# Performance work log

Hardware: AMD Instinct MI355X
Metric: run time of the kernel (lower is better)

Reference implementation:

```python
import jax, jax.numpy as jnp
import numpy as np

B, L, LE = 2, 1024, 1024
NM, DM, NL = 80, 512, 8
LAYERS = NL // 2
DS, EXP, K, H = 16, 2, 4, 4
DI = EXP * DM            # 1024
DTR = (DM + 15) // 16    # dt_rank 'auto' -> 32
HD = DM // H             # 128


def setup_inputs() -> dict:
    key = jax.random.key(0)
    ks = iter(jax.random.split(key, 48))
    n = lambda shape, s=0.02: jax.random.normal(next(ks), shape, jnp.float32) * s
    return {
        "x": jax.random.normal(next(ks), (B, L, NM), jnp.float32),
        "enc_output": jax.random.normal(next(ks), (B, LE, DM), jnp.float32),
        "W_in": n((DM, NM)), "b_in": jnp.zeros((DM,), jnp.float32),
        "m_norm_w": jnp.ones((LAYERS, DM), jnp.float32),
        "m_in_w": n((LAYERS, 2 * DI, DM)),
        "m_conv_w": n((LAYERS, DI, K), 0.1),
        "m_conv_b": jnp.zeros((LAYERS, DI), jnp.float32),
        "m_xproj_w": n((LAYERS, DTR + 2 * DS, DI)),
        "m_dt_w": n((LAYERS, DI, DTR)),
        "m_dt_b": n((LAYERS, DI), 0.1),
        "m_Alog": jnp.tile(jnp.log(jnp.arange(1, DS + 1, dtype=jnp.float32))[None, None, :], (LAYERS, DI, 1)),
        "m_D": jnp.ones((LAYERS, DI), jnp.float32),
        "m_out_w": n((LAYERS, DM, DI)),
        "a_in_w": n((LAYERS, 3 * DM, DM)),
        "a_in_b": jnp.zeros((LAYERS, 3 * DM), jnp.float32),
        "a_out_w": n((LAYERS, DM, DM)),
        "a_out_b": jnp.zeros((LAYERS, DM), jnp.float32),
        "a_ln_w": jnp.ones((LAYERS, DM), jnp.float32),
        "a_ln_b": jnp.zeros((LAYERS, DM), jnp.float32),
        "normf_w": jnp.ones((DM,), jnp.float32),
        "W_out": n((NM, DM)),
    }


def rmsnorm(x, w, eps=1e-5):
    return x * jax.lax.rsqrt(jnp.mean(x * x, axis=-1, keepdims=True) + eps) * w


def layernorm(x, w, b, eps=1e-5):
    m = jnp.mean(x, axis=-1, keepdims=True)
    v = jnp.mean((x - m) ** 2, axis=-1, keepdims=True)
    return (x - m) * jax.lax.rsqrt(v + eps) * w + b


def dwconv_causal(x, w, b):
    # x: (B,L,DI), w: (DI,K) depthwise; torch Conv1d(padding=K-1)[..., :L] == left-pad K-1
    xt = jnp.transpose(x, (0, 2, 1))  # (B,DI,L)
    y = jax.lax.conv_general_dilated(xt, w[:, None, :], (1,), [(K - 1, 0)],
                                     feature_group_count=DI,
                                     dimension_numbers=("NCH", "OIH", "NCH"))
    return jnp.transpose(y, (0, 2, 1)) + b


def selective_scan_cumsum(u, delta, A, Bm, Cm, Dv):
    # mamba-tiny 'cumsum' scan. u,delta: (B,L,DI); A: (DI,DS); Bm,Cm: (B,L,DS); Dv: (DI,)
    dA = jnp.einsum("bld,dn->bldn", delta, A)
    dBu = jnp.einsum("bld,bld,bln->bldn", delta, u, Bm)
    shifted = jnp.pad(dA[:, 1:], ((0, 0), (0, 1), (0, 0), (0, 0)))
    dA_cs = jnp.exp(jnp.flip(jnp.cumsum(jnp.flip(shifted, 1), 1), 1))  # suffix-sum exp
    xs = jnp.cumsum(dBu * dA_cs, axis=1) / (dA_cs + 1e-12)
    y = jnp.einsum("bldn,bln->bld", xs, Cm)
    return y + u * Dv


def mamba_block(u, in_w, conv_w, conv_b, xproj_w, dt_w, dt_b, Alog, Dv, out_w):
    xr = u @ in_w.T                       # (B,L,2*DI)
    xm, res = xr[..., :DI], xr[..., DI:]
    xm = jax.nn.silu(dwconv_causal(xm, conv_w, conv_b))
    x_dbl = xm @ xproj_w.T                # (B,L,DTR+2*DS)
    dlt = x_dbl[..., :DTR]
    Bm = x_dbl[..., DTR:DTR + DS]
    Cm = x_dbl[..., DTR + DS:]
    delta = jax.nn.softplus(dlt @ dt_w.T + dt_b)
    A = -jnp.exp(Alog)
    y = selective_scan_cumsum(xm, delta, A, Bm, Cm, Dv)
    y = y * jax.nn.silu(res)
    return y @ out_w.T


def cross_attn_block(q_in, kv, in_w, in_b, out_w, out_b, ln_w, ln_b):
    Wq, Wk, Wv = in_w[:DM], in_w[DM:2 * DM], in_w[2 * DM:]
    bq, bk, bv = in_b[:DM], in_b[DM:2 * DM], in_b[2 * DM:]
    q = (q_in @ Wq.T + bq).reshape(B, -1, H, HD)
    k = (kv @ Wk.T + bk).reshape(B, -1, H, HD)
    v = (kv @ Wv.T + bv).reshape(B, -1, H, HD)
    scores = jnp.einsum("bqhd,bkhd->bhqk", q, k) / jnp.sqrt(jnp.float32(HD))
    attn = jax.nn.softmax(scores, axis=-1)
    o = jnp.einsum("bhqk,bkhd->bqhd", attn, v).reshape(B, -1, DM)
    o = o @ out_w.T + out_b
    return layernorm(q_in + o, ln_w, ln_b)  # dropout is identity in eval


def reference(x, enc_output, W_in, b_in, m_norm_w, m_in_w, m_conv_w, m_conv_b,
              m_xproj_w, m_dt_w, m_dt_b, m_Alog, m_D, m_out_w,
              a_in_w, a_in_b, a_out_w, a_out_b, a_ln_w, a_ln_b, normf_w, W_out):
    h = x @ W_in.T + b_in
    for i in range(LAYERS):
        h = h + mamba_block(rmsnorm(h, m_norm_w[i]), m_in_w[i], m_conv_w[i],
                            m_conv_b[i], m_xproj_w[i], m_dt_w[i], m_dt_b[i],
                            m_Alog[i], m_D[i], m_out_w[i])
        h = cross_attn_block(h, enc_output, a_in_w[i], a_in_b[i],
                             a_out_w[i], a_out_b[i], a_ln_w[i], a_ln_b[i])
    h = rmsnorm(h, normf_w)
    return h @ W_out.T
```

## Files before the change

### kernel.cpp

```cpp
#include <hip/hip_runtime.h>
#include <hip/hip_bf16.h>
#include <math.h>

typedef __hip_bfloat16 bf16;
typedef __attribute__((ext_vector_type(8))) short short8x;
typedef __attribute__((ext_vector_type(4))) float f32x4;

static constexpr int cB   = 2;
static constexpr int cL   = 1024;
static constexpr int cLE  = 1024;
static constexpr int cNM  = 80;
static constexpr int cDM  = 512;
static constexpr int cLAYERS = 4;
static constexpr int cDS  = 16;
static constexpr int cKC  = 4;
static constexpr int cH   = 4;
static constexpr int cDI  = 1024;
static constexpr int cDTR = 32;
static constexpr int cHD  = 128;

static constexpr int cNCH = 64;
static constexpr int cCHL = cL / cNCH;

#define GLL16(g, l) __builtin_amdgcn_global_load_lds( \
    (const __attribute__((address_space(1))) void*)(g), \
    (__attribute__((address_space(3))) void*)(l), 16, 0, 0)

template<int ACT, int BM, int BN>
__global__ __launch_bounds__(256)
void bgemm_kernel(const bf16* __restrict__ A, const bf16* __restrict__ W,
                  const float* __restrict__ bias, const float* __restrict__ addv,
                  float* __restrict__ Cf, bf16* __restrict__ Cb,
                  int M, int N, int Kd, int lda, int ldw, int ldcf, int ldcb, int ldadd,
                  int bdiv, long sA1, long sA2, long sW1, long sW2,
                  long sCf1, long sCf2, long sCb1, long sCb2)
{
    constexpr int RM = BM / 32;
    constexpr int RN = BN / 32;
    const int z = blockIdx.z;
    const int i1 = z / bdiv, i2 = z % bdiv;
    A += i1 * sA1 + i2 * sA2;
    W += i1 * sW1 + i2 * sW2;

    const int bm = blockIdx.y * BM;
    const int bn = blockIdx.x * BN;
    const int tid = threadIdx.x;
    const int lane = tid & 63;
    const int wid = tid >> 6;
    const int wr = wid >> 1, wc = wid & 1;

    __shared__ bf16 As[BM * 32];
    __shared__ bf16 Bs[BN * 32];

    f32x4 acc[RM][RN] = {};

    const int r_in = lane >> 2;
    const int kb   = (lane & 3) * 8;
    const int hi   = lane >> 4;
    const int rc   = lane & 15;

    for (int k0 = 0; k0 < Kd; k0 += 32) {
#pragma unroll
        for (int iss = 0; iss < BM / 64; iss++) {
            const int row = wid * (BM / 4) + iss * 16 + r_in;
            int gm = bm + row; if (gm >= M) gm = M - 1;
            const bf16* ga = A + (long)gm * lda + k0 + kb;
            GLL16(ga, As + (wid * (BM / 4) + iss * 16) * 32);
        }
#pragma unroll
        for (int iss = 0; iss < BN / 64; iss++) {
            const int row = wid * (BN / 4) + iss * 16 + r_in;
            int gn = bn + row; if (gn >= N) gn = N - 1;
            const bf16* gb = W + (long)gn * ldw + k0 + kb;
            GLL16(gb, Bs + (wid * (BN / 4) + iss * 16) * 32);
        }
        asm volatile("s_waitcnt vmcnt(0)" ::: "memory");
        __syncthreads();

        short8x af[RM], bfv[RN];
#pragma unroll
        for (int i = 0; i < RM; i++)
            af[i] = *(const short8x*)(As + (wr * (BM / 2) + i * 16 + rc) * 32 + hi * 8);
#pragma unroll
        for (int j = 0; j < RN; j++)
            bfv[j] = *(const short8x*)(Bs + (wc * (BN / 2) + j * 16 + rc) * 32 + hi * 8);
#pragma unroll
        for (int i = 0; i < RM; i++)
#pragma unroll
            for (int j = 0; j < RN; j++)
                acc[i][j] = __builtin_amdgcn_mfma_f32_16x16x32_bf16(af[i], bfv[j], acc[i][j], 0, 0, 0);
        __syncthreads();
    }

    const long cfo = i1 * sCf1 + i2 * sCf2;
    const long cbo = i1 * sCb1 + i2 * sCb2;
#pragma unroll
    for (int i = 0; i < RM; i++) {
#pragma unroll
        for (int r = 0; r < 4; r++) {
            const int gm = bm + wr * (BM / 2) + i * 16 + hi * 4 + r;
            if (gm >= M) continue;
#pragma unroll
            for (int j = 0; j < RN; j++) {
                const int gn = bn + wc * (BN / 2) + j * 16 + rc;
                if (gn >= N) continue;
                float v = acc[i][j][r];
                if (bias) v += bias[gn];
                if (ACT == 1) v = (v > 20.f) ? v : log1pf(__expf(v));
                if (addv) v += addv[cfo + (long)gm * ldadd + gn];
                if (Cf) Cf[cfo + (long)gm * ldcf + gn] = v;
                if (Cb) Cb[cbo + (long)gm * ldcb + gn] = __float2bfloat16(v);
            }
        }
    }
}

static inline void bgemm(int ACT, int BM, int BN, const bf16* A, const bf16* W, const float* bias,
                         const float* addv, float* Cf, bf16* Cb,
                         int M, int N, int Kd, int lda, int ldw, int ldcf, int ldcb, int ldadd,
                         int nz, int bdiv, long sA1, long sA2, long sW1, long sW2,
                         long sCf1, long sCf2, long sCb1, long sCb2, hipStream_t s)
{
    dim3 g((N + BN - 1) / BN, (M + BM - 1) / BM, nz), b(256);
#define BG_ARGS A, W, bias, addv, Cf, Cb, M, N, Kd, lda, ldw, ldcf, ldcb, ldadd, \
                bdiv, sA1, sA2, sW1, sW2, sCf1, sCf2, sCb1, sCb2
    if (BM == 128) {
        if (ACT == 1) bgemm_kernel<1, 128, 128><<<g, b, 0, s>>>(BG_ARGS);
        else          bgemm_kernel<0, 128, 128><<<g, b, 0, s>>>(BG_ARGS);
    } else if (BN == 128) {
        if (ACT == 1) bgemm_kernel<1, 64, 128><<<g, b, 0, s>>>(BG_ARGS);
        else          bgemm_kernel<0, 64, 128><<<g, b, 0, s>>>(BG_ARGS);
    } else {
        bgemm_kernel<0, 64, 64><<<g, b, 0, s>>>(BG_ARGS);
    }
#undef BG_ARGS
}

static inline void bgemm_plain(int ACT, int BM, int BN, const bf16* A, const bf16* W,
                               const float* bias, const float* addv, float* Cf, bf16* Cb,
                               int M, int N, int Kd, int lda, int ldw, int ldcf, int ldcb,
                               int ldadd, hipStream_t s)
{
    bgemm(ACT, BM, BN, A, W, bias, addv, Cf, Cb, M, N, Kd, lda, ldw, ldcf, ldcb, ldadd,
          1, 1, 0, 0, 0, 0, 0, 0, 0, 0, s);
}

__global__ __launch_bounds__(128)
void flash_attn_kernel(const bf16* __restrict__ Qp, const bf16* __restrict__ Kp,
                       const bf16* __restrict__ VTp, bf16* __restrict__ Op, float scale)
{
    const int qt = blockIdx.x;
    const int bh = blockIdx.y;
    const int b = bh >> 2, h = bh & 3;
    const int tid = threadIdx.x;
    const int w = tid >> 6;
    const int lane = tid & 63;
    const int rc = lane & 15, hi = lane >> 4;
    const int rlo = rc & 7;

    __shared__ bf16 Qs[32 * 128];
    __shared__ bf16 Ks[64 * 128];
    __shared__ bf16 Vs[128 * 64];
    __shared__ bf16 Ps[32 * 64];

    {
        const bf16* qb = Qp + ((long)(b * cL + qt * 32)) * cDM + h * cHD;
#pragma unroll
        for (int c = 0; c < 4; c++) {
            const int row = w * 16 + c * 4 + (lane >> 4);
            const int gc = (lane & 15) ^ (row & 7);
            GLL16(qb + (long)row * cDM + gc * 8, Qs + (w * 16 + c * 4) * 128);
        }
    }
    asm volatile("s_waitcnt vmcnt(0)" ::: "memory");
    __syncthreads();

    short8x aq[4];
#pragma unroll
    for (int kk = 0; kk < 4; kk++) {
        const int sc = (kk * 4 + hi) ^ rlo;
        aq[kk] = *(const short8x*)(Qs + (w * 16 + rc) * 128 + sc * 8);
    }

    float m_r[4], l_r[4];
#pragma unroll
    for (int r = 0; r < 4; r++) { m_r[r] = -1e30f; l_r[r] = 0.f; }
    f32x4 oacc[8] = {};

    const bf16* kb0 = Kp + ((long)(b * cLE)) * (2 * cDM) + h * cHD;
    const bf16* vb0 = VTp + ((long)(b * cDM + h * cHD)) * cLE;

    for (int kt = 0; kt < 16; kt++) {
        __syncthreads();
#pragma unroll
        for (int c = 0; c < 8; c++) {
            const int row = w * 32 + c * 4 + (lane >> 4);
            const int gc = (lane & 15) ^ (row & 7);
            GLL16(kb0 + ((long)(kt * 64 + row)) * (2 * cDM) + gc * 8,
                  Ks + (w * 32 + c * 4) * 128);
        }
#pragma unroll
        for (int c = 0; c < 8; c++) {
            const int row = w * 64 + c * 8 + (lane >> 3);
            const int gc = (lane & 7) ^ (row & 7);
            GLL16(vb0 + (long)row * cLE + kt * 64 + gc * 8,
                  Vs + (w * 64 + c * 8) * 64);
        }
        asm volatile("s_waitcnt vmcnt(0)" ::: "memory");
        __syncthreads();

        f32x4 s[4] = {};
#pragma unroll
        for (int kk = 0; kk < 4; kk++) {
            const int sc = (kk * 4 + hi) ^ rlo;
#pragma unroll
            for (int j = 0; j < 4; j++) {
                short8x bk = *(const short8x*)(Ks + (j * 16 + rc) * 128 + sc * 8);
                s[j] = __builtin_amdgcn_mfma_f32_16x16x32_bf16(aq[kk], bk, s[j], 0, 0, 0);
            }
        }

        float p[4][4];
        float esc[4];
#pragma unroll
        for (int r = 0; r < 4; r++) {
            const float v0 = s[0][r] * scale, v1 = s[1][r] * scale;
            const float v2 = s[2][r] * scale, v3 = s[3][r] * scale;
            float mx = fmaxf(fmaxf(v0, v1), fmaxf(v2, v3));
            mx = fmaxf(mx, __shfl_xor(mx, 1));
            mx = fmaxf(mx, __shfl_xor(mx, 2));
            mx = fmaxf(mx, __shfl_xor(mx, 4));
            mx = fmaxf(mx, __shfl_xor(mx, 8));
            const float mn = fmaxf(m_r[r], mx);
            p[0][r] = __expf(v0 - mn);
            p[1][r] = __expf(v1 - mn);
            p[2][r] = __expf(v2 - mn);
            p[3][r] = __expf(v3 - mn);
            float rs = (p[0][r] + p[1][r]) + (p[2][r] + p[3][r]);
            rs += __shfl_xor(rs, 1);
            rs += __shfl_xor(rs, 2);
            rs += __shfl_xor(rs, 4);
            rs += __shfl_xor(rs, 8);
            esc[r] = __expf(m_r[r] - mn);
            l_r[r] = l_r[r] * esc[r] + rs;
            m_r[r] = mn;
        }
#pragma unroll
        for (int j2 = 0; j2 < 8; j2++)
#pragma unroll
            for (int r = 0; r < 4; r++)
                oacc[j2][r] *= esc[r];
#pragma unroll
        for (int j = 0; j < 4; j++)
#pragma unroll
            for (int r = 0; r < 4; r++) {
                const int q = w * 16 + hi * 4 + r;
                const int cp = (j * 2 + (rc >> 3)) ^ (q & 7);
                Ps[q * 64 + cp * 8 + (rc & 7)] = __float2bfloat16(p[j][r]);
            }
        __syncthreads();
#pragma unroll
        for (int ks = 0; ks < 2; ks++) {
            const int sc = (ks * 4 + hi) ^ rlo;
            short8x ap = *(const short8x*)(Ps + (w * 16 + rc) * 64 + sc * 8);
#pragma unroll
            for (int j2 = 0; j2 < 8; j2++) {
                short8x bv = *(const short8x*)(Vs + (j2 * 16 + rc) * 64 + sc * 8);
                oacc[j2] = __builtin_amdgcn_mfma_f32_16x16x32_bf16(ap, bv, oacc[j2], 0, 0, 0);
            }
        }
    }

    float inv[4];
#pragma unroll
    for (int r = 0; r < 4; r++) inv[r] = 1.f / l_r[r];
    bf16* ob = Op + ((long)(b * cL + qt * 32)) * cDM + h * cHD;
#pragma unroll
    for (int j2 = 0; j2 < 8; j2++)
#pragma unroll
        for (int r = 0; r < 4; r++)
            ob[(long)(w * 16 + hi * 4 + r) * cDM + j2 * 16 + rc] =
                __float2bfloat16(oacc[j2][r] * inv[r]);
}

__global__ void splitk_reduce_kernel(const float* __restrict__ parts, float* __restrict__ outf,
                                     bf16* __restrict__ outb, int n4, int sliceN4, int S)
{
    const int i = blockIdx.x * 256 + threadIdx.x;
    if (i >= n4) return;
    float4 a = ((const float4*)parts)[i];
    for (int s2 = 1; s2 < S; s2++) {
        float4 b2 = ((const float4*)parts)[i + (long)s2 * sliceN4];
        a.x += b2.x; a.y += b2.y; a.z += b2.z; a.w += b2.w;
    }
    ((float4*)outf)[i] = a;
    bf16 b0 = __float2bfloat16(a.x), b1 = __float2bfloat16(a.y);
    bf16 b2 = __float2bfloat16(a.z), b3 = __float2bfloat16(a.w);
    short4 pk = { *(short*)&b0, *(short*)&b1, *(short*)&b2, *(short*)&b3 };
    ((short4*)outb)[i] = pk;
}

__global__ void f32_to_bf16_kernel(const float* __restrict__ in, bf16* __restrict__ out, long n)
{
    long i = ((long)blockIdx.x * 256 + threadIdx.x) * 4;
    if (i + 3 < n) {
        float4 v = *(const float4*)(in + i);
        out[i]     = __float2bfloat16(v.x);
        out[i + 1] = __float2bfloat16(v.y);
        out[i + 2] = __float2bfloat16(v.z);
        out[i + 3] = __float2bfloat16(v.w);
    } else {
        for (; i < n; i++) out[i] = __float2bfloat16(in[i]);
    }
}
static inline void cvt(const float* in, bf16* out, long n, hipStream_t s)
{
    int blocks = (int)((n / 4 + 255) / 256);
    f32_to_bf16_kernel<<<blocks, 256, 0, s>>>(in, out, n);
}

__global__ void cvt_pad_kernel(const float* __restrict__ in, bf16* __restrict__ out,
                               int rows, int kin, int kout)
{
    const int idx = blockIdx.x * 256 + threadIdx.x;
    if (idx >= rows * kout) return;
    const int r = idx / kout, k = idx - r * kout;
    out[idx] = __float2bfloat16(k < kin ? in[(long)r * kin + k] : 0.f);
}

__global__ void transpose_bf16_kernel(const bf16* __restrict__ in, bf16* __restrict__ out,
                                      int ldin, int col0)
{
    __shared__ bf16 t[32][33];
    const int b = blockIdx.z;
    const int le0 = blockIdx.x * 32, d0 = blockIdx.y * 32;
    const int tid = threadIdx.x;
    const int c = tid & 31, r = tid >> 5;
    for (int i = r; i < 32; i += 8)
        t[i][c] = in[((long)b * cLE + le0 + i) * ldin + col0 + d0 + c];
    __syncthreads();
    for (int i = r; i < 32; i += 8)
        out[((long)b * cDM + d0 + i) * cLE + le0 + c] = t[c][i];
}

__global__ void rmsnorm_kernel(const float* __restrict__ x, const float* __restrict__ w,
                               float* __restrict__ outf, bf16* __restrict__ outb, int Dm)
{
    const int row = blockIdx.x;
    const float* xr = x + (long)row * Dm;
    float s = 0.f;
    for (int i = threadIdx.x; i < Dm; i += 256) { float v = xr[i]; s += v * v; }
    __shared__ float red[5];
    const int lane = threadIdx.x & 63, wv = threadIdx.x >> 6;
#pragma unroll
    for (int off = 1; off < 64; off <<= 1) s += __shfl_xor(s, off);
    if (lane == 0) red[wv] = s;
    __syncthreads();
    if (threadIdx.x == 0) {
        float t = red[0] + red[1] + red[2] + red[3];
        red[4] = rsqrtf(t / Dm + 1e-5f);
    }
    __syncthreads();
    const float scale = red[4];
    for (int i = threadIdx.x; i < Dm; i += 256) {
        float v = xr[i] * scale * w[i];
        if (outf) outf[(long)row * Dm + i] = v;
        if (outb) outb[(long)row * Dm + i] = __float2bfloat16(v);
    }
}

__global__ void layernorm_kernel(const float* __restrict__ x, const float* __restrict__ w,
                                 const float* __restrict__ b, float* __restrict__ outf,
                                 bf16* __restrict__ outb, int Dm)
{
    const int row = blockIdx.x;
    const float* xr = x + (long)row * Dm;
    float s = 0.f, sq = 0.f;
    for (int i = threadIdx.x; i < Dm; i += 256) { float v = xr[i]; s += v; sq += v * v; }
    __shared__ float red[8];
    __shared__ float mv[2];
    const int lane = threadIdx.x & 63, wv = threadIdx.x >> 6;
#pragma unroll
    for (int off = 1; off < 64; off <<= 1) { s += __shfl_xor(s, off); sq += __shfl_xor(sq, off); }
    if (lane == 0) { red[wv] = s; red[4 + wv] = sq; }
    __syncthreads();
    if (threadIdx.x == 0) {
        float ts = red[0] + red[1] + red[2] + red[3];
        float tq = red[4] + red[5] + red[6] + red[7];
        float m = ts / Dm;
        float var = tq / Dm - m * m;
        mv[0] = m;
        mv[1] = rsqrtf(var + 1e-5f);
    }
    __syncthreads();
    const float m = mv[0], rs = mv[1];
    for (int i = threadIdx.x; i < Dm; i += 256) {
        float v = (xr[i] - m) * rs * w[i] + b[i];
        outf[(long)row * Dm + i] = v;
        outb[(long)row * Dm + i] = __float2bfloat16(v);
    }
}

__global__ void conv_silu_kernel(const float* __restrict__ xr, const float* __restrict__ w,
                                 const float* __restrict__ bias, float* __restrict__ xm,
                                 bf16* __restrict__ xmb)
{
    const int idx = blockIdx.x * 256 + threadIdx.x;
    if (idx >= cB * cL * cDI) return;
    const int d = idx & (cDI - 1);
    const int l = (idx >> 10) & (cL - 1);
    const int b = idx >> 20;
    float s = bias[d];
#pragma unroll
    for (int j = 0; j < cKC; j++) {
        const int ls = l + j - (cKC - 1);
        if (ls >= 0) s += w[d * cKC + j] * xr[((long)(b * cL + ls)) * (2 * cDI) + d];
    }
    s = s / (1.f + __expf(-s));
    xm[(long)idx] = s;
    xmb[(long)idx] = __float2bfloat16(s);
}

__global__ void scan_phase1(const float* __restrict__ xm, const float* __restrict__ delta,
                            const float* __restrict__ xdbl, const float* __restrict__ Alog,
                            float* __restrict__ aprod_out, float* __restrict__ send_out)
{
    const int idx4 = blockIdx.x * 256 + threadIdx.x;
    const int ng = idx4 & 3;
    const int d  = (idx4 >> 2) & (cDI - 1);
    const int ch = (idx4 >> 12) & (cNCH - 1);
    const int b  = idx4 >> 18;
    const float4 Al = *(const float4*)(Alog + d * cDS + 4 * ng);
    const float A0 = -__expf(Al.x), A1 = -__expf(Al.y), A2 = -__expf(Al.z), A3 = -__expf(Al.w);
    float s0 = 0.f, s1 = 0.f, s2 = 0.f, s3 = 0.f;
    float p0 = 1.f, p1 = 1.f, p2 = 1.f, p3 = 1.f;
    const int l0 = ch * cCHL;
    const float* dp = delta + (long)(b * cL + l0) * cDI + d;
    const float* up = xm    + (long)(b * cL + l0) * cDI + d;
    const float* xb = xdbl  + (long)(b * cL + l0) * 64 + cDTR + 4 * ng;
#pragma unroll
    for (int t = 0; t < cCHL; t++) {
        const float dl = dp[(long)t * cDI];
        const float du = dl * up[(long)t * cDI];
        const float4 Bv = *(const float4*)(xb + (long)t * 64);
        const float a0 = __expf(dl * A0), a1 = __expf(dl * A1);
        const float a2 = __expf(dl * A2), a3 = __expf(dl * A3);
        s0 = a0 * s0 + du * Bv.x; p0 *= a0;
        s1 = a1 * s1 + du * Bv.y; p1 *= a1;
        s2 = a2 * s2 + du * Bv.z; p2 *= a2;
        s3 = a3 * s3 + du * Bv.w; p3 *= a3;
    }
    const long base4 = (((long)(b * cNCH + ch) * cDI + d) * cDS) + 4 * ng;
    float4 pv = { p0, p1, p2, p3 };
    float4 sv = { s0, s1, s2, s3 };
    *(float4*)(aprod_out + base4) = pv;
    *(float4*)(send_out + base4)  = sv;
}

__global__ void scan_phase2(const float* __restrict__ aprod, const float* __restrict__ send,
                            float* __restrict__ sinit)
{
    const int j = blockIdx.x * 256 + threadIdx.x;
    const int n = j & (cDS - 1);
    const int d = (j >> 4) & (cDI - 1);
    const int b = j >> 14;
    float s = 0.f;
#pragma unroll
    for (int c = 0; c < cNCH; c++) {
        const long off = (((long)(b * cNCH + c) * cDI + d) * cDS) + n;
        sinit[off] = s;
        s = aprod[off] * s + send[off];
    }
}

__global__ void scan_phase3(const float* __restrict__ xm, const float* __restrict__ delta,
                            const float* __restrict__ xdbl, const float* __restrict__ Alog,
                            const float* __restrict__ Dv, const float* __restrict__ xr,
                            const float* __restrict__ sinit, bf16* __restrict__ y)
{
    const int idx4 = blockIdx.x * 256 + threadIdx.x;
    const int ng = idx4 & 3;
    const int d  = (idx4 >> 2) & (cDI - 1);
    const int ch = (idx4 >> 12) & (cNCH - 1);
    const int b  = idx4 >> 18;
    const float4 Al = *(const float4*)(Alog + d * cDS + 4 * ng);
    const float A0 = -__expf(Al.x), A1 = -__expf(Al.y), A2 = -__expf(Al.z), A3 = -__expf(Al.w);
    const float Dval = Dv[d];
    const long base4 = (((long)(b * cNCH + ch) * cDI + d) * cDS) + 4 * ng;
    float4 st = *(const float4*)(sinit + base4);
    float s0 = st.x, s1 = st.y, s2 = st.z, s3 = st.w;
    const int l0 = ch * cCHL;
    const float* dp = delta + (long)(b * cL + l0) * cDI + d;
    const float* up = xm    + (long)(b * cL + l0) * cDI + d;
    const float* xb = xdbl  + (long)(b * cL + l0) * 64 + cDTR + 4 * ng;
    const float* xc = xb + cDS;
    const float* rp = xr + (long)(b * cL + l0) * (2 * cDI) + cDI + d;
    bf16* yp = y + (long)(b * cL + l0) * cDI + d;
#pragma unroll
    for (int t = 0; t < cCHL; t++) {
        const float dl = dp[(long)t * cDI];
        const float u  = up[(long)t * cDI];
        const float du = dl * u;
        const float4 Bv = *(const float4*)(xb + (long)t * 64);
        const float4 Cv = *(const float4*)(xc + (long)t * 64);
        const float a0 = __expf(dl * A0), a1 = __expf(dl * A1);
        const float a2 = __expf(dl * A2), a3 = __expf(dl * A3);
        s0 = a0 * s0 + du * Bv.x;
        s1 = a1 * s1 + du * Bv.y;
        s2 = a2 * s2 + du * Bv.z;
        s3 = a3 * s3 + du * Bv.w;
        float c = s0 * Cv.x;
        c = fmaf(s1, Cv.y, c);
        c = fmaf(s2, Cv.z, c);
        c = fmaf(s3, Cv.w, c);
        c += __shfl_xor(c, 1);
        c += __shfl_xor(c, 2);
        if (ng == 0) {
            const float res = rp[(long)t * 2 * cDI];
            const float sig = 1.f / (1.f + __expf(-res));
            yp[(long)t * cDI] = __float2bfloat16((c + u * Dval) * (res * sig));
        }
    }
}

extern "C" void kernel_launch(void* const* d_in, const int* in_sizes, int n_in,
                              void* d_out, int out_size, void* d_ws, size_t ws_size,
                              hipStream_t stream)
{
    const float* x       = (const float*)d_in[0];
    const float* enc     = (const float*)d_in[1];
    const float* W_in    = (const float*)d_in[2];
    const float* b_in    = (const float*)d_in[3];
    const float* m_norm_w= (const float*)d_in[4];
    const float* m_in_w  = (const float*)d_in[5];
    const float* m_conv_w= (const float*)d_in[6];
    const float* m_conv_b= (const float*)d_in[7];
    const float* m_xproj = (const float*)d_in[8];
    const float* m_dt_w  = (const float*)d_in[9];
    const float* m_dt_b  = (const float*)d_in[10];
    const float* m_Alog  = (const float*)d_in[11];
    const float* m_D     = (const float*)d_in[12];
    const float* m_out_w = (const float*)d_in[13];
    const float* a_in_w  = (const float*)d_in[14];
    const float* a_in_b  = (const float*)d_in[15];
    const float* a_out_w = (const float*)d_in[16];
    const float* a_out_b = (const float*)d_in[17];
    const float* a_ln_w  = (const float*)d_in[18];
    const float* a_ln_b  = (const float*)d_in[19];
    const float* normf_w = (const float*)d_in[20];
    const float* W_out   = (const float*)d_in[21];
    float* out = (float*)d_out;

    float* ws = (float*)d_ws;
    long off = 0;
    auto allocf = [&](long n) { float* p = ws + off; off += n; return p; };

    const long M1 = 1 << 20;
    float* bufH    = allocf(M1);
    float* bufPre  = allocf(M1);
    float* bufXR   = allocf(4 * M1);
    float* bufXM   = allocf(2 * M1);
    float* bufDelta= allocf(2 * M1);
    float* bufXDBL = allocf(M1 / 8);
    bf16* bufU    = (bf16*)allocf(M1 / 2);
    bf16* bufHb   = (bf16*)allocf(M1 / 2);
    bf16* bufXMb  = (bf16*)allocf(M1);
    bf16* bufXDBLb= (bf16*)allocf(M1 / 16);
    bf16* bufY    = (bf16*)allocf(M1);
    bf16* bufQ    = (bf16*)allocf(M1 / 2);
    bf16* bufKV   = (bf16*)allocf(M1);
    bf16* bufVT   = (bf16*)allocf(M1 / 2);
    bf16* bufO    = (bf16*)allocf(M1 / 2);
    bf16* encb    = (bf16*)allocf(M1 / 2);
    bf16* w_in_b  = (bf16*)allocf(2 * M1);
    bf16* w_xp_b  = (bf16*)allocf(M1 / 8);
    bf16* w_dt_b  = (bf16*)allocf(M1 / 16);
    bf16* w_out_b = (bf16*)allocf(M1);
    bf16* w_ain_b = (bf16*)allocf(3 * M1 / 2);
    bf16* w_aout_b= (bf16*)allocf(M1 / 2);
    bf16* x_pad   = (bf16*)allocf(2048L * 96 / 2);
    bf16* w_inp_b = (bf16*)allocf(512L * 96 / 2);
    bf16* w_outf_b= (bf16*)allocf(80L * 512 / 2);
    float* bufAP  = allocf(2 * M1);
    float* bufSE  = allocf(2 * M1);
    float* bufSI  = allocf(2 * M1);

    const int Mrows = cB * cL;
    const long SUMSZ4 = (long)cB * cNCH * cDI * 4;

    cvt(enc,      encb,    (long)cB * cLE * cDM, stream);
    cvt(m_in_w,   w_in_b,  (long)cLAYERS * 2 * cDI * cDM, stream);
    cvt(m_xproj,  w_xp_b,  (long)cLAYERS * 64 * cDI, stream);
    cvt(m_dt_w,   w_dt_b,  (long)cLAYERS * cDI * cDTR, stream);
    cvt(m_out_w,  w_out_b, (long)cLAYERS * cDM * cDI, stream);
    cvt(a_in_w,   w_ain_b, (long)cLAYERS * 3 * cDM * cDM, stream);
    cvt(a_out_w,  w_aout_b,(long)cLAYERS * cDM * cDM, stream);
    cvt(W_out,    w_outf_b,(long)cNM * cDM, stream);
    cvt_pad_kernel<<<(Mrows * 96 + 255) / 256, 256, 0, stream>>>(x, x_pad, Mrows, cNM, 96);
    cvt_pad_kernel<<<(cDM * 96 + 255) / 256, 256, 0, stream>>>(W_in, w_inp_b, cDM, cNM, 96);

    bgemm_plain(0, 64, 64, x_pad, w_inp_b, b_in, nullptr, bufH, nullptr,
                Mrows, cDM, 96, 96, 96, cDM, 0, 0, stream);

    for (int i = 0; i < cLAYERS; i++) {
        const float* norm_w = m_norm_w + (long)i * cDM;
        const bf16*  in_w   = w_in_b   + (long)i * 2 * cDI * cDM;
        const float* conv_w = m_conv_w + (long)i * cDI * cKC;
        const float* conv_b = m_conv_b + (long)i * cDI;
        const bf16*  xproj  = w_xp_b   + (long)i * 64 * cDI;
        const bf16*  dt_w   = w_dt_b   + (long)i * cDI * cDTR;
        const float* dt_b   = m_dt_b   + (long)i * cDI;
        const float* Alog   = m_Alog   + (long)i * cDI * cDS;
        const float* Dv     = m_D      + (long)i * cDI;
        const bf16*  out_w  = w_out_b  + (long)i * cDM * cDI;
        const bf16*  ain_w  = w_ain_b  + (long)i * 3 * cDM * cDM;
        const float* ain_b  = a_in_b   + (long)i * 3 * cDM;
        const bf16*  aout_w = w_aout_b + (long)i * cDM * cDM;
        const float* aout_b = a_out_b  + (long)i * cDM;
        const float* ln_w   = a_ln_w   + (long)i * cDM;
        const float* ln_b   = a_ln_b   + (long)i * cDM;

        rmsnorm_kernel<<<Mrows, 256, 0, stream>>>(bufH, norm_w, nullptr, bufU, cDM);
        bgemm_plain(0, 64, 128, bufU, in_w, nullptr, nullptr, bufXR, nullptr,
                    Mrows, 2 * cDI, cDM, cDM, cDM, 2 * cDI, 0, 0, stream);
        conv_silu_kernel<<<(cB * cL * cDI) / 256, 256, 0, stream>>>(bufXR, conv_w, conv_b, bufXM, bufXMb);
        bgemm(0, 64, 64, bufXMb, xproj, nullptr, nullptr, bufPre, nullptr,
              Mrows, 64, cDI / 8, cDI, cDI, 64, 0, 0,
              8, 1, 128, 0, 128, 0, (long)Mrows * 64, 0, 0, 0, stream);
        splitk_reduce_kernel<<<(Mrows * 64 / 4 + 255) / 256, 256, 0, stream>>>(
            bufPre, bufXDBL, bufXDBLb, Mrows * 64 / 4, Mrows * 64 / 4, 8);
        bgemm_plain(1, 64, 128, bufXDBLb, dt_w, dt_b, nullptr, bufDelta, nullptr,
                    Mrows, cDI, cDTR, 64, cDTR, cDI, 0, 0, stream);
        scan_phase1<<<(int)(SUMSZ4 / 256), 256, 0, stream>>>(bufXM, bufDelta, bufXDBL, Alog, bufAP, bufSE);
        scan_phase2<<<(cB * cDI * cDS) / 256, 256, 0, stream>>>(bufAP, bufSE, bufSI);
        scan_phase3<<<(int)(SUMSZ4 / 256), 256, 0, stream>>>(bufXM, bufDelta, bufXDBL, Alog, Dv, bufXR, bufSI, bufY);
        bgemm_plain(0, 64, 64, bufY, out_w, nullptr, bufH, bufH, bufHb,
                    Mrows, cDM, cDI, cDI, cDI, cDM, cDM, cDM, stream);

        bgemm_plain(0, 64, 64, bufHb, ain_w, ain_b, nullptr, nullptr, bufQ,
                    Mrows, cDM, cDM, cDM, cDM, 0, cDM, 0, stream);
        bgemm_plain(0, 64, 128, encb, ain_w + (long)cDM * cDM, ain_b + cDM, nullptr, nullptr, bufKV,
                    Mrows, 2 * cDM, cDM, cDM, cDM, 0, 2 * cDM, 0, stream);
        {
            dim3 g(cLE / 32, cDM / 32, cB);
            transpose_bf16_kernel<<<g, 256, 0, stream>>>(bufKV, bufVT, 2 * cDM, cDM);
        }
        {
            dim3 g(cL / 32, cB * cH);
            flash_attn_kernel<<<g, 128, 0, stream>>>(bufQ, bufKV, bufVT, bufO,
                                                     0.08838834764831845f);
        }
        bgemm_plain(0, 64, 64, bufO, aout_w, aout_b, bufH, bufPre, nullptr,
                    Mrows, cDM, cDM, cDM, cDM, cDM, 0, cDM, stream);
        layernorm_kernel<<<Mrows, 256, 0, stream>>>(bufPre, ln_w, ln_b, bufH, bufHb, cDM);
    }

    rmsnorm_kernel<<<Mrows, 256, 0, stream>>>(bufH, normf_w, nullptr, bufU, cDM);
    bgemm_plain(0, 64, 64, bufU, w_outf_b, nullptr, nullptr, out, nullptr,
                Mrows, cNM, cDM, cDM, cDM, cNM, 0, 0, stream);
}
```

Before: 858.7 us.

## Batch K/V projections for all layers upfront and merge weight conversions

```diff
diff --git a/kernel.cpp b/kernel.cpp
--- a/kernel.cpp
+++ b/kernel.cpp
@@ -33,7 +33,7 @@
                   float* __restrict__ Cf, bf16* __restrict__ Cb,
                   int M, int N, int Kd, int lda, int ldw, int ldcf, int ldcb, int ldadd,
                   int bdiv, long sA1, long sA2, long sW1, long sW2,
-                  long sCf1, long sCf2, long sCb1, long sCb2)
+                  long sCf1, long sCf2, long sCb1, long sCb2, long sBias)
 {
     constexpr int RM = BM / 32;
     constexpr int RN = BN / 32;
@@ -41,6 +41,7 @@
     const int i1 = z / bdiv, i2 = z % bdiv;
     A += i1 * sA1 + i2 * sA2;
     W += i1 * sW1 + i2 * sW2;
+    if (bias) bias += i1 * sBias;
 
     const int bm = blockIdx.y * BM;
     const int bn = blockIdx.x * BN;
@@ -119,11 +120,11 @@
                          const float* addv, float* Cf, bf16* Cb,
                          int M, int N, int Kd, int lda, int ldw, int ldcf, int ldcb, int ldadd,
                          int nz, int bdiv, long sA1, long sA2, long sW1, long sW2,
-                         long sCf1, long sCf2, long sCb1, long sCb2, hipStream_t s)
+                         long sCf1, long sCf2, long sCb1, long sCb2, long sBias, hipStream_t s)
 {
     dim3 g((N + BN - 1) / BN, (M + BM - 1) / BM, nz), b(256);
 #define BG_ARGS A, W, bias, addv, Cf, Cb, M, N, Kd, lda, ldw, ldcf, ldcb, ldadd, \
-                bdiv, sA1, sA2, sW1, sW2, sCf1, sCf2, sCb1, sCb2
+                bdiv, sA1, sA2, sW1, sW2, sCf1, sCf2, sCb1, sCb2, sBias
     if (BM == 128) {
         if (ACT == 1) bgemm_kernel<1, 128, 128><<<g, b, 0, s>>>(BG_ARGS);
         else          bgemm_kernel<0, 128, 128><<<g, b, 0, s>>>(BG_ARGS);
@@ -142,7 +143,7 @@
                                int ldadd, hipStream_t s)
 {
     bgemm(ACT, BM, BN, A, W, bias, addv, Cf, Cb, M, N, Kd, lda, ldw, ldcf, ldcb, ldadd,
-          1, 1, 0, 0, 0, 0, 0, 0, 0, 0, s);
+          1, 1, 0, 0, 0, 0, 0, 0, 0, 0, 0, s);
 }
 
 __global__ __launch_bounds__(128)
@@ -300,23 +301,36 @@
     ((short4*)outb)[i] = pk;
 }
 
-__global__ void f32_to_bf16_kernel(const float* __restrict__ in, bf16* __restrict__ out, long n)
-{
+__global__ void cvt_all_kernel(
+    const float* __restrict__ s0, bf16* __restrict__ d0,
+    const float* __restrict__ s1, bf16* __restrict__ d1,
+    const float* __restrict__ s2, bf16* __restrict__ d2,
+    const float* __restrict__ s3, bf16* __restrict__ d3,
+    const float* __restrict__ s4, bf16* __restrict__ d4,
+    const float* __restrict__ s5, bf16* __restrict__ d5,
+    const float* __restrict__ s6, bf16* __restrict__ d6,
+    const float* __restrict__ s7, bf16* __restrict__ d7)
+{
+    constexpr long E0 = 1048576, E1 = 4194304, E2 = 262144, E3 = 131072;
+    constexpr long E4 = 2097152, E5 = 3145728, E6 = 1048576, E7 = 40960;
+    constexpr long C0 = E0, C1 = C0 + E1, C2 = C1 + E2, C3 = C2 + E3;
+    constexpr long C4 = C3 + E4, C5 = C4 + E5, C6 = C5 + E6, C7 = C6 + E7;
     long i = ((long)blockIdx.x * 256 + threadIdx.x) * 4;
-    if (i + 3 < n) {
-        float4 v = *(const float4*)(in + i);
-        out[i]     = __float2bfloat16(v.x);
-        out[i + 1] = __float2bfloat16(v.y);
-        out[i + 2] = __float2bfloat16(v.z);
-        out[i + 3] = __float2bfloat16(v.w);
-    } else {
-        for (; i < n; i++) out[i] = __float2bfloat16(in[i]);
-    }
-}
-static inline void cvt(const float* in, bf16* out, long n, hipStream_t s)
-{
-    int blocks = (int)((n / 4 + 255) / 256);
-    f32_to_bf16_kernel<<<blocks, 256, 0, s>>>(in, out, n);
+    if (i >= C7) return;
+    const float* s; bf16* d;
+    if      (i < C0) { s = s0; d = d0; }
+    else if (i < C1) { s = s1; d = d1; i -= C0; }
+    else if (i < C2) { s = s2; d = d2; i -= C1; }
+    else if (i < C3) { s = s3; d = d3; i -= C2; }
+    else if (i < C4) { s = s4; d = d4; i -= C3; }
+    else if (i < C5) { s = s5; d = d5; i -= C4; }
+    else if (i < C6) { s = s6; d = d6; i -= C5; }
+    else             { s = s7; d = d7; i -= C6; }
+    float4 v = *(const float4*)(s + i);
+    d[i]     = __float2bfloat16(v.x);
+    d[i + 1] = __float2bfloat16(v.y);
+    d[i + 2] = __float2bfloat16(v.z);
+    d[i + 3] = __float2bfloat16(v.w);
 }
 
 __global__ void cvt_pad_kernel(const float* __restrict__ in, bf16* __restrict__ out,
@@ -329,10 +343,13 @@
 }
 
 __global__ void transpose_bf16_kernel(const bf16* __restrict__ in, bf16* __restrict__ out,
-                                      int ldin, int col0)
+                                      int ldin, int col0, long inLS, long outLS)
 {
     __shared__ bf16 t[32][33];
-    const int b = blockIdx.z;
+    const int z = blockIdx.z;
+    const int lay = z >> 1, b = z & 1;
+    in  += (long)lay * inLS;
+    out += (long)lay * outLS;
     const int le0 = blockIdx.x * 32, d0 = blockIdx.y * 32;
     const int tid = threadIdx.x;
     const int c = tid & 31, r = tid >> 5;
@@ -568,8 +585,6 @@
     bf16* bufXDBLb= (bf16*)allocf(M1 / 16);
     bf16* bufY    = (bf16*)allocf(M1);
     bf16* bufQ    = (bf16*)allocf(M1 / 2);
-    bf16* bufKV   = (bf16*)allocf(M1);
-    bf16* bufVT   = (bf16*)allocf(M1 / 2);
     bf16* bufO    = (bf16*)allocf(M1 / 2);
     bf16* encb    = (bf16*)allocf(M1 / 2);
     bf16* w_in_b  = (bf16*)allocf(2 * M1);
@@ -584,20 +599,32 @@
     float* bufAP  = allocf(2 * M1);
     float* bufSE  = allocf(2 * M1);
     float* bufSI  = allocf(2 * M1);
+    bf16* bufKV4  = (bf16*)allocf(4 * M1);
+    bf16* bufVT4  = (bf16*)allocf(2 * M1);
 
     const int Mrows = cB * cL;
     const long SUMSZ4 = (long)cB * cNCH * cDI * 4;
-
-    cvt(enc,      encb,    (long)cB * cLE * cDM, stream);
-    cvt(m_in_w,   w_in_b,  (long)cLAYERS * 2 * cDI * cDM, stream);
-    cvt(m_xproj,  w_xp_b,  (long)cLAYERS * 64 * cDI, stream);
-    cvt(m_dt_w,   w_dt_b,  (long)cLAYERS * cDI * cDTR, stream);
-    cvt(m_out_w,  w_out_b, (long)cLAYERS * cDM * cDI, stream);
-    cvt(a_in_w,   w_ain_b, (long)cLAYERS * 3 * cDM * cDM, stream);
-    cvt(a_out_w,  w_aout_b,(long)cLAYERS * cDM * cDM, stream);
-    cvt(W_out,    w_outf_b,(long)cNM * cDM, stream);
+    const long kvLS = (long)Mrows * 2 * cDM;
+    const long vtLS = (long)cB * cDM * cLE;
+
+    cvt_all_kernel<<<11688, 256, 0, stream>>>(
+        enc, encb, m_in_w, w_in_b, m_xproj, w_xp_b, m_dt_w, w_dt_b,
+        m_out_w, w_out_b, a_in_w, w_ain_b, a_out_w, w_aout_b, W_out, w_outf_b);
     cvt_pad_kernel<<<(Mrows * 96 + 255) / 256, 256, 0, stream>>>(x, x_pad, Mrows, cNM, 96);
     cvt_pad_kernel<<<(cDM * 96 + 255) / 256, 256, 0, stream>>>(W_in, w_inp_b, cDM, cNM, 96);
+
+    bgemm(0, 64, 128, encb, w_ain_b + (long)cDM * cDM, a_in_b + cDM, nullptr, nullptr, bufKV4,
+          Mrows, 2 * cDM, cDM, cDM, cDM, 0, 2 * cDM, 0,
+          cLAYERS, 1,
+          0, 0,
+          (long)3 * cDM * cDM, 0,
+          0, 0, kvLS, 0,
+          (long)3 * cDM,
+          stream);
+    {
+        dim3 g(cLE / 32, cDM / 32, cLAYERS * cB);
+        transpose_bf16_kernel<<<g, 256, 0, stream>>>(bufKV4, bufVT4, 2 * cDM, cDM, kvLS, vtLS);
+    }
 
     bgemm_plain(0, 64, 64, x_pad, w_inp_b, b_in, nullptr, bufH, nullptr,
                 Mrows, cDM, 96, 96, 96, cDM, 0, 0, stream);
@@ -619,6 +646,8 @@
         const float* aout_b = a_out_b  + (long)i * cDM;
         const float* ln_w   = a_ln_w   + (long)i * cDM;
         const float* ln_b   = a_ln_b   + (long)i * cDM;
+        const bf16*  kv_l   = bufKV4 + (long)i * kvLS;
+        const bf16*  vt_l   = bufVT4 + (long)i * vtLS;
 
         rmsnorm_kernel<<<Mrows, 256, 0, stream>>>(bufH, norm_w, nullptr, bufU, cDM);
         bgemm_plain(0, 64, 128, bufU, in_w, nullptr, nullptr, bufXR, nullptr,
@@ -626,7 +655,7 @@
         conv_silu_kernel<<<(cB * cL * cDI) / 256, 256, 0, stream>>>(bufXR, conv_w, conv_b, bufXM, bufXMb);
         bgemm(0, 64, 64, bufXMb, xproj, nullptr, nullptr, bufPre, nullptr,
               Mrows, 64, cDI / 8, cDI, cDI, 64, 0, 0,
-              8, 1, 128, 0, 128, 0, (long)Mrows * 64, 0, 0, 0, stream);
+              8, 1, 128, 0, 128, 0, (long)Mrows * 64, 0, 0, 0, 0, stream);
         splitk_reduce_kernel<<<(Mrows * 64 / 4 + 255) / 256, 256, 0, stream>>>(
             bufPre, bufXDBL, bufXDBLb, Mrows * 64 / 4, Mrows * 64 / 4, 8);
         bgemm_plain(1, 64, 128, bufXDBLb, dt_w, dt_b, nullptr, bufDelta, nullptr,
@@ -639,15 +668,9 @@
 
         bgemm_plain(0, 64, 64, bufHb, ain_w, ain_b, nullptr, nullptr, bufQ,
                     Mrows, cDM, cDM, cDM, cDM, 0, cDM, 0, stream);
-        bgemm_plain(0, 64, 128, encb, ain_w + (long)cDM * cDM, ain_b + cDM, nullptr, nullptr, bufKV,
-                    Mrows, 2 * cDM, cDM, cDM, cDM, 0, 2 * cDM, 0, stream);
-        {
-            dim3 g(cLE / 32, cDM / 32, cB);
-            transpose_bf16_kernel<<<g, 256, 0, stream>>>(bufKV, bufVT, 2 * cDM, cDM);
-        }
         {
             dim3 g(cL / 32, cB * cH);
-            flash_attn_kernel<<<g, 128, 0, stream>>>(bufQ, bufKV, bufVT, bufO,
+            flash_attn_kernel<<<g, 128, 0, stream>>>(bufQ, kv_l, vt_l, bufO,
                                                      0.08838834764831845f);
         }
         bgemm_plain(0, 64, 64, bufO, aout_w, aout_b, bufH, bufPre, nullptr,
```

New measurement: 797.4 us. 7.1% less time.
